# Performance work log

Measured on AMD Instinct MI355X. Metric: run time of the kernel, lower is better.

Reference implementation:

```python
import jax, jax.numpy as jnp
import numpy as np

B, S, H, E, K = 8, 4096, 1024, 256, 64
NEG = -1e30  # finite stand-in for -inf to keep grads NaN-free


def setup_inputs() -> dict:
    key = jax.random.key(0)
    ks = jax.random.split(key, 8)
    Hq = H // 4
    sc = 0.02
    return {
        "hidden_states": jax.random.normal(ks[0], (B, S, H), dtype=jnp.float32),
        "attention_mask": jnp.ones((B, S), dtype=jnp.int32),
        "block_boundaries": jnp.sort(jax.random.randint(ks[1], (B, K), 0, S), axis=-1),
        "tok_w1": jax.random.normal(ks[2], (H, Hq), dtype=jnp.float32) * sc,
        "tok_b1": jnp.zeros((Hq,), dtype=jnp.float32),
        "tok_w2": jax.random.normal(ks[3], (Hq, 1), dtype=jnp.float32) * sc,
        "tok_b2": jnp.zeros((1,), dtype=jnp.float32),
        "blk_w1": jax.random.normal(ks[4], (H, Hq), dtype=jnp.float32) * sc,
        "blk_b1": jnp.zeros((Hq,), dtype=jnp.float32),
        "blk_w2": jax.random.normal(ks[5], (Hq, 1), dtype=jnp.float32) * sc,
        "blk_b2": jnp.zeros((1,), dtype=jnp.float32),
        "out_w": jax.random.normal(ks[6], (H, E), dtype=jnp.float32) * sc,
        "out_b": jnp.zeros((E,), dtype=jnp.float32),
    }


def _attn_scores(x, w1, b1, w2, b2):
    # Linear -> Tanh -> Linear(.,1), squeeze last dim
    return (jnp.tanh(x @ w1 + b1) @ w2 + b2)[..., 0]


def reference(hidden_states, attention_mask, block_boundaries,
              tok_w1, tok_b1, tok_w2, tok_b2,
              blk_w1, blk_b1, blk_w2, blk_b2,
              out_w, out_b):
    Bz, Sz, Hz = hidden_states.shape
    Kz = block_boundaries.shape[1]
    pos = jnp.arange(Sz)
    # token -> block id: last boundary <= pos (tokens before first boundary get -1)
    block_id = jax.vmap(lambda bnd: jnp.searchsorted(bnd, pos, side='right') - 1)(block_boundaries)  # [B,S]
    member = block_id[:, :, None] == jnp.arange(Kz)[None, None, :]      # [B,S,K]
    valid = (attention_mask == 1) & (block_id >= 0)                     # [B,S]
    m_full = member & valid[:, :, None]                                 # [B,S,K]

    # stage 1: per-block masked softmax over tokens
    tok_scores = _attn_scores(hidden_states, tok_w1, tok_b1, tok_w2, tok_b2)  # [B,S]
    s = jnp.where(m_full, tok_scores[:, :, None], NEG)
    mx = jnp.max(s, axis=1, keepdims=True)                              # [B,1,K]
    e = jnp.where(m_full, jnp.exp(tok_scores[:, :, None] - mx), 0.0)
    denom = jnp.sum(e, axis=1, keepdims=True)                           # [B,1,K]
    w = jnp.where(denom > 0, e / jnp.maximum(denom, 1e-30), 0.0)
    block_embed = jnp.einsum('bsk,bsd->bkd', w, hidden_states)          # [B,K,H]
    block_valid = denom[:, 0, :] > 0                                    # [B,K] (empty blocks dropped)

    # stage 2: softmax over (non-empty) blocks
    blk_scores = _attn_scores(block_embed, blk_w1, blk_b1, blk_w2, blk_b2)    # [B,K]
    blk_scores = jnp.where(block_valid, blk_scores, NEG)
    bw = jax.nn.softmax(blk_scores, axis=-1)
    func = jnp.einsum('bk,bkd->bd', bw, block_embed)                    # [B,H]

    out = func @ out_w + out_b                                          # [B,E]
    return out / jnp.maximum(jnp.linalg.norm(out, axis=-1, keepdims=True), 1e-12)
```

## Files before the change

### kernel.cpp

```cpp
#include <hip/hip_runtime.h>
#include <math.h>
#include <limits.h>

#define BB 8
#define SS 4096
#define HH 1024
#define EE 256
#define KK 64
#define HQ 256
#define NEGF -1e30f

typedef short bf16x8 __attribute__((ext_vector_type(8)));
typedef float f32x4  __attribute__((ext_vector_type(4)));

__device__ inline short f2bf(float x) {
    unsigned u = __float_as_uint(x);
    unsigned r = (u + 0x7fffu + ((u >> 16) & 1u)) >> 16;
    return (short)r;
}

__device__ inline unsigned pk2bf(float lo, float hi) {
    unsigned a = __float_as_uint(lo) + 0x8000u;
    unsigned b = __float_as_uint(hi) + 0x8000u;
    return (a >> 16) | (b & 0xffff0000u);
}

__global__ __launch_bounds__(256) void convert_both_kernel(
    const float* __restrict__ tok_w1, const float* __restrict__ blk_w1,
    short* __restrict__ w1s_tok, short* __restrict__ w1s_blk)
{
    const int kb = blockIdx.x & 31, which = blockIdx.x >> 5;
    const float* src = which ? blk_w1 : tok_w1;
    short* dst = which ? w1s_blk : w1s_tok;
    const int n = threadIdx.x;
    for (int kk = 0; kk < 32; kk++)
        dst[kb * 8192 + n * 32 + kk] = f2bf(src[(kb * 32 + kk) * HQ + n]);
}

__global__ __launch_bounds__(256, 4) void mfma_score4_kernel(
    const float* __restrict__ X, const short* __restrict__ w1s,
    const float* __restrict__ b1, const float* __restrict__ w2,
    const float* __restrict__ b2, float* __restrict__ out)
{
    __shared__ __attribute__((aligned(16))) short As[2][4][1024];
    __shared__ float part[4][32];

    const int t = threadIdx.x;
    const int wv = t >> 6, lane = t & 63, lo = lane & 15, q = lane >> 4;
    const long row0 = (long)blockIdx.x * 32;

    f32x4 acc[2][4];
#pragma unroll
    for (int i = 0; i < 2; i++)
#pragma unroll
        for (int j = 0; j < 4; j++) acc[i][j] = (f32x4){0.f, 0.f, 0.f, 0.f};

    const int c = t >> 1, half = t & 1;
    const int srow = ((c >> 6) << 4) + (c & 15);
    const int skofs = ((c >> 4) & 3) * 8 + half * 4;
    const float* xs = X + (row0 + srow) * HH + skofs;
    const int dofs = c * 8 + half * 4;
    const short* wp = w1s + (wv * 64 + lo) * 32 + q * 8;

    float4 sv[4];
    bf16x8 bC[4], bN[4];

#pragma unroll
    for (int j = 0; j < 4; j++) sv[j] = *(const float4*)(xs + j * 32);
#pragma unroll
    for (int j = 0; j < 4; j++) {
        unsigned u0 = pk2bf(sv[j].x, sv[j].y), u1 = pk2bf(sv[j].z, sv[j].w);
        unsigned* d = (unsigned*)&As[0][j][dofs];
        d[0] = u0; d[1] = u1;
    }
#pragma unroll
    for (int j = 0; j < 4; j++) sv[j] = *(const float4*)(xs + (4 + j) * 32);
#pragma unroll
    for (int ct = 0; ct < 4; ct++) bC[ct] = *(const bf16x8*)(wp + ct * 512);
    asm volatile("s_waitcnt lgkmcnt(0)" ::: "memory");
    __builtin_amdgcn_sched_barrier(0);
    __builtin_amdgcn_s_barrier();
    __builtin_amdgcn_sched_barrier(0);

#define KSTEP(J, BUSE, BPRE, KBN)                                              \
    {                                                                          \
        _Pragma("unroll")                                                      \
        for (int ct = 0; ct < 4; ct++)                                         \
            BPRE[ct] = *(const bf16x8*)(wp + (KBN) * 8192 + ct * 512);         \
        bf16x8 af0 = *(const bf16x8*)&As[cur][J][(q * 16 + lo) * 8];           \
        bf16x8 af1 = *(const bf16x8*)&As[cur][J][(64 + q * 16 + lo) * 8];      \
        _Pragma("unroll")                                                      \
        for (int ct = 0; ct < 4; ct++) {                                       \
            acc[0][ct] = __builtin_amdgcn_mfma_f32_16x16x32_bf16(              \
                af0, BUSE[ct], acc[0][ct], 0, 0, 0);                           \
            acc[1][ct] = __builtin_amdgcn_mfma_f32_16x16x32_bf16(              \
                af1, BUSE[ct], acc[1][ct], 0, 0, 0);                           \
        }                                                                      \
    }

    for (int ci = 0; ci < 8; ci++) {
        const int cur = ci & 1;
        const int kb0 = ci * 4;
        KSTEP(0, bC, bN, kb0 + 1)
        KSTEP(1, bN, bC, kb0 + 2)
        KSTEP(2, bC, bN, kb0 + 3)
        const int kbn3 = (kb0 + 4 < 32) ? kb0 + 4 : 31;
        KSTEP(3, bN, bC, kbn3)
        if (ci < 7) {
#pragma unroll
            for (int j = 0; j < 4; j++) {
                unsigned u0 = pk2bf(sv[j].x, sv[j].y), u1 = pk2bf(sv[j].z, sv[j].w);
                unsigned* d = (unsigned*)&As[cur ^ 1][j][dofs];
                d[0] = u0; d[1] = u1;
            }
            const int cn = (ci + 2 < 8) ? ci + 2 : 7;
#pragma unroll
            for (int j = 0; j < 4; j++)
                sv[j] = *(const float4*)(xs + (cn * 4 + j) * 32);
        }
        asm volatile("s_waitcnt lgkmcnt(0)" ::: "memory");
        __builtin_amdgcn_sched_barrier(0);
        __builtin_amdgcn_s_barrier();
        __builtin_amdgcn_sched_barrier(0);
    }
#undef KSTEP

    float rowpart[2][4];
#pragma unroll
    for (int rt = 0; rt < 2; rt++)
#pragma unroll
        for (int r = 0; r < 4; r++) rowpart[rt][r] = 0.f;
#pragma unroll
    for (int ct = 0; ct < 4; ct++) {
        const int cc = wv * 64 + ct * 16 + lo;
        const float b1c = b1[cc], w2c = w2[cc];
#pragma unroll
        for (int rt = 0; rt < 2; rt++)
#pragma unroll
            for (int r = 0; r < 4; r++)
                rowpart[rt][r] += tanhf(acc[rt][ct][r] + b1c) * w2c;
    }
#pragma unroll
    for (int rt = 0; rt < 2; rt++)
#pragma unroll
        for (int r = 0; r < 4; r++) {
            float v = rowpart[rt][r];
            v += __shfl_down(v, 8, 64);
            v += __shfl_down(v, 4, 64);
            v += __shfl_down(v, 2, 64);
            v += __shfl_down(v, 1, 64);
            rowpart[rt][r] = v;
        }
    if (lo == 0)
#pragma unroll
        for (int rt = 0; rt < 2; rt++)
#pragma unroll
            for (int r = 0; r < 4; r++)
                part[wv][rt * 16 + q * 4 + r] = rowpart[rt][r];
    __syncthreads();
    if (t < 32)
        out[row0 + t] = part[0][t] + part[1][t] + part[2][t] + part[3][t] + b2[0];
}

__global__ __launch_bounds__(256) void block_stats_kernel(
    const float* __restrict__ scores, const int* __restrict__ mask,
    const int* __restrict__ bnd, float* __restrict__ bden,
    float* __restrict__ wtok, float* __restrict__ embed)
{
    const int b = blockIdx.x >> 6, k = blockIdx.x & 63;
    const int start = bnd[b * KK + k];
    const int end = (k == KK - 1) ? SS : bnd[b * KK + k + 1];
    const int tid = threadIdx.x;
    __shared__ float r[4];
    __shared__ float mshared, dshared;

    *((float4*)(embed + (long)blockIdx.x * HH) + tid) = (float4){0.f, 0.f, 0.f, 0.f};
    if (k == 0)
        for (int s = tid; s < start; s += 256) wtok[b * SS + s] = 0.f;

    float m = NEGF;
    for (int s = start + tid; s < end; s += 256)
        if (mask[b * SS + s] == 1) m = fmaxf(m, scores[b * SS + s]);
    for (int off = 32; off > 0; off >>= 1) m = fmaxf(m, __shfl_down(m, off, 64));
    if ((tid & 63) == 0) r[tid >> 6] = m;
    __syncthreads();
    if (tid == 0) mshared = fmaxf(fmaxf(r[0], r[1]), fmaxf(r[2], r[3]));
    __syncthreads();
    m = mshared;

    float d = 0.f;
    for (int s = start + tid; s < end; s += 256)
        if (mask[b * SS + s] == 1) d += expf(scores[b * SS + s] - m);
    for (int off = 32; off > 0; off >>= 1) d += __shfl_down(d, off, 64);
    __syncthreads();
    if ((tid & 63) == 0) r[tid >> 6] = d;
    __syncthreads();
    if (tid == 0) {
        float den = r[0] + r[1] + r[2] + r[3];
        bden[blockIdx.x] = den;
        dshared = (den > 0.f) ? 1.f / fmaxf(den, 1e-30f) : 0.f;
    }
    __syncthreads();
    const float inv = dshared;
    for (int s = start + tid; s < end; s += 256)
        wtok[b * SS + s] = (mask[b * SS + s] == 1) ? expf(scores[b * SS + s] - m) * inv : 0.f;
}

#define TCH 16
__global__ __launch_bounds__(256) void block_embed4_kernel(
    const float* __restrict__ hidden, const float* __restrict__ wtok,
    const int* __restrict__ bnd, float* __restrict__ embed)
{
    const int b = blockIdx.x >> 8;
    const int ch = blockIdx.x & 255;
    const int t = threadIdx.x;
    __shared__ int bsh[KK];
    __shared__ float wsh[TCH];
    const int s0 = ch * TCH, s1 = s0 + TCH;
    if (t < KK) bsh[t] = bnd[b * KK + t];
    if (t >= 64 && t < 64 + TCH) wsh[t - 64] = wtok[b * SS + s0 + (t - 64)];
    __syncthreads();

    int cur = -1;
#pragma unroll
    for (int i = 0; i < KK; i++) cur = (bsh[i] <= s0) ? i : cur;
    const int nxt = (cur + 1 < KK) ? bsh[cur + 1] : INT_MAX;

    const float* hr0 = hidden + ((long)b * SS + s0) * HH + t;
    float a0 = 0.f, a1 = 0.f, a2 = 0.f, a3 = 0.f;

    if (nxt >= s1 && cur >= 0) {
#pragma unroll
        for (int i = 0; i < TCH; i++) {
            const float w = wsh[i];
            const float* hr = hr0 + (long)i * HH;
            a0 = fmaf(w, hr[0], a0);
            a1 = fmaf(w, hr[256], a1);
            a2 = fmaf(w, hr[512], a2);
            a3 = fmaf(w, hr[768], a3);
        }
        float* e = embed + ((long)b * KK + cur) * HH;
        atomicAdd(e + t, a0); atomicAdd(e + t + 256, a1);
        atomicAdd(e + t + 512, a2); atomicAdd(e + t + 768, a3);
        return;
    }

    bool any = false;
    for (int s = s0; s < s1; s++) {
        while (cur + 1 < KK && bsh[cur + 1] <= s) {
            if (any) {
                float* e = embed + ((long)b * KK + cur) * HH;
                atomicAdd(e + t, a0); atomicAdd(e + t + 256, a1);
                atomicAdd(e + t + 512, a2); atomicAdd(e + t + 768, a3);
                a0 = a1 = a2 = a3 = 0.f; any = false;
            }
            cur++;
        }
        if (cur < 0) continue;
        const float w = wsh[s - s0];
        const float* hr = hr0 + (long)(s - s0) * HH;
        a0 = fmaf(w, hr[0], a0);
        a1 = fmaf(w, hr[256], a1);
        a2 = fmaf(w, hr[512], a2);
        a3 = fmaf(w, hr[768], a3);
        any = true;
    }
    if (any) {
        float* e = embed + ((long)b * KK + cur) * HH;
        atomicAdd(e + t, a0); atomicAdd(e + t + 256, a1);
        atomicAdd(e + t + 512, a2); atomicAdd(e + t + 768, a3);
    }
}

__global__ __launch_bounds__(256) void finalize_ab_kernel(
    const float* __restrict__ embed, const float* __restrict__ bscores,
    const float* __restrict__ bden, const float* __restrict__ out_w,
    float* __restrict__ osum)
{
    const int b = blockIdx.x >> 5;
    const int hc = (blockIdx.x >> 2) & 7;
    const int hq = blockIdx.x & 3;
    const int t = threadIdx.x;
    __shared__ float bw[KK];
    __shared__ float fpart[8][32];
    __shared__ float fsh[32];

    if (t < KK) {
        float s = (bden[b * KK + t] > 0.f) ? bscores[b * KK + t] : NEGF;
        float m = s;
        for (int off = 32; off > 0; off >>= 1) m = fmaxf(m, __shfl_xor(m, off, 64));
        float e = expf(s - m);
        float d = e;
        for (int off = 32; off > 0; off >>= 1) d += __shfl_xor(d, off, 64);
        bw[t] = e / d;
    }
    __syncthreads();

    const int hbase = hc * 128 + hq * 32;
    {
        const int hh = t & 31, kh = t >> 5;
        const float* ep = embed + ((long)b * KK + kh * 8) * HH + hbase + hh;
        float f = 0.f;
#pragma unroll
        for (int k2 = 0; k2 < 8; k2++)
            f = fmaf(bw[kh * 8 + k2], ep[(long)k2 * HH], f);
        fpart[kh][hh] = f;
    }
    __syncthreads();
    if (t < 32) {
        float f = 0.f;
#pragma unroll
        for (int g = 0; g < 8; g++) f += fpart[g][t];
        fsh[t] = f;
    }
    __syncthreads();

    float acc = 0.f;
    const float* wpp = out_w + (long)hbase * EE + t;
#pragma unroll
    for (int h = 0; h < 32; h++)
        acc = fmaf(fsh[h], wpp[(long)h * EE], acc);
    osum[(long)(b * 32 + hc * 4 + hq) * EE + t] = acc;
}

__global__ __launch_bounds__(256) void finalize_c_kernel(
    const float* __restrict__ osum, const float* __restrict__ out_b,
    float* __restrict__ outp)
{
    const int b = blockIdx.x, t = threadIdx.x;
    __shared__ float r4[4];
    float o = out_b[t];
#pragma unroll
    for (int hc = 0; hc < 32; hc++)
        o += osum[(long)(b * 32 + hc) * EE + t];
    float sq = o * o;
    for (int off = 32; off > 0; off >>= 1) sq += __shfl_down(sq, off, 64);
    if ((t & 63) == 0) r4[t >> 6] = sq;
    __syncthreads();
    const float nrm = sqrtf(r4[0] + r4[1] + r4[2] + r4[3]);
    outp[b * EE + t] = o / fmaxf(nrm, 1e-12f);
}

extern "C" void kernel_launch(void* const* d_in, const int* in_sizes, int n_in,
                              void* d_out, int out_size, void* d_ws, size_t ws_size,
                              hipStream_t stream) {
    const float* hidden  = (const float*)d_in[0];
    const int*   mask    = (const int*)  d_in[1];
    const int*   bnd     = (const int*)  d_in[2];
    const float* tok_w1  = (const float*)d_in[3];
    const float* tok_b1  = (const float*)d_in[4];
    const float* tok_w2  = (const float*)d_in[5];
    const float* tok_b2  = (const float*)d_in[6];
    const float* blk_w1  = (const float*)d_in[7];
    const float* blk_b1  = (const float*)d_in[8];
    const float* blk_w2  = (const float*)d_in[9];
    const float* blk_b2  = (const float*)d_in[10];
    const float* out_w   = (const float*)d_in[11];
    const float* out_b   = (const float*)d_in[12];

    float* ws      = (float*)d_ws;
    float* wtok    = ws;
    float* embed   = ws + 32768;
    float* scores  = ws + 557056;
    float* bden    = ws + 589824;
    float* bscores = ws + 590336;
    float* osum    = ws + 590848;
    short* w1s_tok = (short*)(ws + 656384);
    short* w1s_blk = w1s_tok + 262144;

    convert_both_kernel<<<64, 256, 0, stream>>>(tok_w1, blk_w1, w1s_tok, w1s_blk);
    mfma_score4_kernel<<<BB * SS / 32, 256, 0, stream>>>(
        hidden, w1s_tok, tok_b1, tok_w2, tok_b2, scores);
    block_stats_kernel<<<BB * KK, 256, 0, stream>>>(
        scores, mask, bnd, bden, wtok, embed);
    block_embed4_kernel<<<BB * SS / TCH, 256, 0, stream>>>(hidden, wtok, bnd, embed);
    mfma_score4_kernel<<<BB * KK / 32, 256, 0, stream>>>(
        embed, w1s_blk, blk_b1, blk_w2, blk_b2, bscores);
    finalize_ab_kernel<<<BB * 32, 256, 0, stream>>>(
        embed, bscores, bden, out_w, osum);
    finalize_c_kernel<<<BB, 256, 0, stream>>>(osum, out_b, (float*)d_out);
}
```

Before: 291.1 us.

## Compute block embeddings per block directly instead of chunked atomics

Replaces the token-chunk kernel that scattered partial sums into embeddings with atomics by a kernel that assigns one workgroup per (batch, block, quarter of hidden dim) and sums over that block's tokens directly. This removes the atomics and the zero-init of embeddings in the stats kernel. The trade-off is load imbalance: block lengths vary with the random boundaries, so long blocks serialize on few workgroups with only 2048 workgroups total. Tokens before the first boundary are skipped, which is correct since their weights are zero.

```diff
diff --git a/kernel.cpp b/kernel.cpp
--- a/kernel.cpp
+++ b/kernel.cpp
@@ -165,7 +165,7 @@
 __global__ __launch_bounds__(256) void block_stats_kernel(
     const float* __restrict__ scores, const int* __restrict__ mask,
     const int* __restrict__ bnd, float* __restrict__ bden,
-    float* __restrict__ wtok, float* __restrict__ embed)
+    float* __restrict__ wtok)
 {
     const int b = blockIdx.x >> 6, k = blockIdx.x & 63;
     const int start = bnd[b * KK + k];
@@ -174,7 +174,6 @@
     __shared__ float r[4];
     __shared__ float mshared, dshared;
 
-    *((float4*)(embed + (long)blockIdx.x * HH) + tid) = (float4){0.f, 0.f, 0.f, 0.f};
     if (k == 0)
         for (int s = tid; s < start; s += 256) wtok[b * SS + s] = 0.f;
 
@@ -206,70 +205,38 @@
         wtok[b * SS + s] = (mask[b * SS + s] == 1) ? expf(scores[b * SS + s] - m) * inv : 0.f;
 }
 
-#define TCH 16
-__global__ __launch_bounds__(256) void block_embed4_kernel(
+__global__ __launch_bounds__(256) void block_embed_direct_kernel(
     const float* __restrict__ hidden, const float* __restrict__ wtok,
     const int* __restrict__ bnd, float* __restrict__ embed)
 {
-    const int b = blockIdx.x >> 8;
-    const int ch = blockIdx.x & 255;
+    const int bk = blockIdx.x >> 2;
+    const int hq = blockIdx.x & 3;
+    const int b = bk >> 6, k = bk & 63;
+    const int start = bnd[bk];
+    const int end = (k == KK - 1) ? SS : bnd[bk + 1];
+    const int n = end - start;
     const int t = threadIdx.x;
-    __shared__ int bsh[KK];
-    __shared__ float wsh[TCH];
-    const int s0 = ch * TCH, s1 = s0 + TCH;
-    if (t < KK) bsh[t] = bnd[b * KK + t];
-    if (t >= 64 && t < 64 + TCH) wsh[t - 64] = wtok[b * SS + s0 + (t - 64)];
-    __syncthreads();
-
-    int cur = -1;
-#pragma unroll
-    for (int i = 0; i < KK; i++) cur = (bsh[i] <= s0) ? i : cur;
-    const int nxt = (cur + 1 < KK) ? bsh[cur + 1] : INT_MAX;
-
-    const float* hr0 = hidden + ((long)b * SS + s0) * HH + t;
-    float a0 = 0.f, a1 = 0.f, a2 = 0.f, a3 = 0.f;
-
-    if (nxt >= s1 && cur >= 0) {
-#pragma unroll
-        for (int i = 0; i < TCH; i++) {
-            const float w = wsh[i];
-            const float* hr = hr0 + (long)i * HH;
-            a0 = fmaf(w, hr[0], a0);
-            a1 = fmaf(w, hr[256], a1);
-            a2 = fmaf(w, hr[512], a2);
-            a3 = fmaf(w, hr[768], a3);
-        }
-        float* e = embed + ((long)b * KK + cur) * HH;
-        atomicAdd(e + t, a0); atomicAdd(e + t + 256, a1);
-        atomicAdd(e + t + 512, a2); atomicAdd(e + t + 768, a3);
-        return;
-    }
-
-    bool any = false;
-    for (int s = s0; s < s1; s++) {
-        while (cur + 1 < KK && bsh[cur + 1] <= s) {
-            if (any) {
-                float* e = embed + ((long)b * KK + cur) * HH;
-                atomicAdd(e + t, a0); atomicAdd(e + t + 256, a1);
-                atomicAdd(e + t + 512, a2); atomicAdd(e + t + 768, a3);
-                a0 = a1 = a2 = a3 = 0.f; any = false;
-            }
-            cur++;
-        }
-        if (cur < 0) continue;
-        const float w = wsh[s - s0];
-        const float* hr = hr0 + (long)(s - s0) * HH;
-        a0 = fmaf(w, hr[0], a0);
-        a1 = fmaf(w, hr[256], a1);
-        a2 = fmaf(w, hr[512], a2);
-        a3 = fmaf(w, hr[768], a3);
-        any = true;
-    }
-    if (any) {
-        float* e = embed + ((long)b * KK + cur) * HH;
-        atomicAdd(e + t, a0); atomicAdd(e + t + 256, a1);
-        atomicAdd(e + t + 512, a2); atomicAdd(e + t + 768, a3);
-    }
+    const int col = hq * 256 + t;
+
+    const float* hp = hidden + ((long)b * SS + start) * HH + col;
+    const float* wp = wtok + b * SS + start;
+
+    float acc = 0.f;
+    int s = 0;
+    for (; s + 4 <= n; s += 4) {
+        const float w0 = wp[s],     w1 = wp[s + 1];
+        const float w2 = wp[s + 2], w3 = wp[s + 3];
+        const float h0 = hp[(long)s * HH],      h1 = hp[(long)(s + 1) * HH];
+        const float h2 = hp[(long)(s + 2) * HH], h3 = hp[(long)(s + 3) * HH];
+        acc = fmaf(w0, h0, acc);
+        acc = fmaf(w1, h1, acc);
+        acc = fmaf(w2, h2, acc);
+        acc = fmaf(w3, h3, acc);
+    }
+    for (; s < n; s++)
+        acc = fmaf(wp[s], hp[(long)s * HH], acc);
+
+    embed[(long)bk * HH + col] = acc;
 }
 
 __global__ __launch_bounds__(256) void finalize_ab_kernel(
@@ -372,8 +339,9 @@
     mfma_score4_kernel<<<BB * SS / 32, 256, 0, stream>>>(
         hidden, w1s_tok, tok_b1, tok_w2, tok_b2, scores);
     block_stats_kernel<<<BB * KK, 256, 0, stream>>>(
-        scores, mask, bnd, bden, wtok, embed);
-    block_embed4_kernel<<<BB * SS / TCH, 256, 0, stream>>>(hidden, wtok, bnd, embed);
+        scores, mask, bnd, bden, wtok);
+    block_embed_direct_kernel<<<BB * KK * 4, 256, 0, stream>>>(
+        hidden, wtok, bnd, embed);
     mfma_score4_kernel<<<BB * KK / 32, 256, 0, stream>>>(
         embed, w1s_blk, blk_b1, blk_w2, blk_b2, bscores);
     finalize_ab_kernel<<<BB * 32, 256, 0, stream>>>(
```

Result: slower. 299.3 us (+2.8%).
